# Kernel optimization log

Hardware: AMD Instinct MI355X
Metric: run time of the kernel (lower is better)

## Reference

```python
import jax, jax.numpy as jnp
import numpy as np

N, C, D = 32, 512, 2048
Q = 64          # num_query_tokens
H = 16          # num_attention_heads
DH = D // H     # head dim


def _mlp(z, w1, b1, w2, b2):
    # projection: Linear(D_r -> D_h), GELU (exact erf, torch default), Linear(D_h -> D_h)
    h = jax.nn.gelu(z @ w1 + b1, approximate=False)
    return h @ w2 + b2


def setup_inputs() -> dict:
    key = jax.random.key(0)
    ks = jax.random.split(key, 16)
    s = 0.02
    inp = {
        "x": jax.random.normal(ks[0], (N, C, D), dtype=jnp.float32),
        # projection MLP (shared by both experts since projector_type has no 'proj')
        "proj_w1": jax.random.normal(ks[1], (D, D), dtype=jnp.float32) * s,
        "proj_b1": jnp.zeros((D,), dtype=jnp.float32),
        "proj_w2": jax.random.normal(ks[2], (D, D), dtype=jnp.float32) * s,
        "proj_b2": jnp.zeros((D,), dtype=jnp.float32),
        # TextResampler (cross-attention with learned queries)
        "query_tokens": jax.random.normal(ks[3], (Q, D), dtype=jnp.float32) * s,
        "wq": jax.random.normal(ks[4], (D, D), dtype=jnp.float32) * s,
        "bq": jnp.zeros((D,), dtype=jnp.float32),
        "wk": jax.random.normal(ks[5], (D, D), dtype=jnp.float32) * s,
        "bk": jnp.zeros((D,), dtype=jnp.float32),
        "wv": jax.random.normal(ks[6], (D, D), dtype=jnp.float32) * s,
        "bv": jnp.zeros((D,), dtype=jnp.float32),
        "wo": jax.random.normal(ks[7], (D, D), dtype=jnp.float32) * s,
        "bo": jnp.zeros((D,), dtype=jnp.float32),
        # gate weight (zeros-init in module; random here to exercise routing)
        "w_gate": jax.random.normal(ks[8], (D, 2), dtype=jnp.float32) * s,
    }
    return inp


def reference(x, proj_w1, proj_b1, proj_w2, proj_b2, query_tokens,
              wq, bq, wk, bk, wv, bv, wo, bo, w_gate):
    n, c, d = x.shape
    # --- sampler: AdaptiveAvgPool2d((Q, D)); D dim is identity, C -> Q block means ---
    x_sampler = x.reshape(n, Q, c // Q, d).mean(axis=2)  # [N, Q, D]

    # --- expert 0: projection MLP on pooled tokens ---
    e0 = _mlp(x_sampler, proj_w1, proj_b1, proj_w2, proj_b2)  # [N, Q, D]

    # --- expert 1: TextResampler cross-attention over x, then shared projection ---
    q = (query_tokens @ wq + bq).reshape(Q, H, DH)            # [Q, H, DH]
    k = (x @ wk + bk).reshape(n, c, H, DH)                    # [N, C, H, DH]
    v = (x @ wv + bv).reshape(n, c, H, DH)
    scores = jnp.einsum("qhd,nchd->nhqc", q, k) / jnp.sqrt(jnp.float32(DH))
    attn = jax.nn.softmax(scores, axis=-1)                    # [N, H, Q, C]
    ctx = jnp.einsum("nhqc,nchd->nqhd", attn, v).reshape(n, Q, d)
    resampled = ctx @ wo + bo                                 # [N, Q, D]
    e1 = _mlp(resampled, proj_w1, proj_b1, proj_w2, proj_b2)  # [N, Q, D]

    # --- noisy top-k gating (eval path: clean logits) ---
    flat = x_sampler.reshape(n * Q, d)
    logits = jax.nn.softmax(flat @ w_gate, axis=1)            # [T, 2]
    top_vals, top_idx = jax.lax.top_k(logits, 2)              # min(k+1, num_experts)=2
    top_k_gates = top_vals / (top_vals.sum(axis=1, keepdims=True) + 1e-6)
    gates = jnp.zeros_like(logits).at[
        jnp.arange(n * Q)[:, None], top_idx].set(top_k_gates)
    gates = gates.reshape(n, Q, 2)

    # --- combine: matmul(stack(experts,-1), gates.unsqueeze(-1)).squeeze(-1) ---
    stacked = jnp.stack([e0, e1], axis=-1)                    # [N, Q, D, E]
    out = jnp.einsum("nqde,nqe->nqd", stacked, gates)
    return out.reshape(-1, d)                                 # [N*Q, D]
```

## Files before the change

kernel.cpp:

```cpp
#include <hip/hip_runtime.h>
#include <hip/hip_bf16.h>

typedef float f32x4 __attribute__((ext_vector_type(4)));
typedef short s16x8 __attribute__((ext_vector_type(8)));
typedef __hip_bfloat16 bf16;

#define NB 32
#define CB 512
#define DB 2048
#define QB 64
#define HB 16
#define DHB 128

static __device__ __forceinline__ void gload16(const void* g, void* l) {
  __builtin_amdgcn_global_load_lds(
      (const __attribute__((address_space(1))) void*)g,
      (__attribute__((address_space(3))) void*)l, 16, 0, 0);
}

static __device__ __forceinline__ unsigned short f2bf(float f) {
  bf16 b = __float2bfloat16(f);
  return *reinterpret_cast<unsigned short*>(&b);
}

static __device__ __forceinline__ float gelu_f(float z) {
  return 0.5f * z * (1.0f + erff(z * 0.7071067811865475f));
}

#define BARX do { asm volatile("s_waitcnt lgkmcnt(0)" ::: "memory"); __builtin_amdgcn_s_barrier(); asm volatile("" ::: "memory"); } while (0)
#define VM8  asm volatile("s_waitcnt vmcnt(8)" ::: "memory")
#define VM2  asm volatile("s_waitcnt vmcnt(2)" ::: "memory")

__global__ void k_convpool(const float* __restrict__ x, bf16* __restrict__ x_bf,
                           bf16* __restrict__ xs) {
  const int d0 = blockIdx.x * 512 + threadIdx.x * 2;
  const int q = blockIdx.y, n = blockIdx.z;
  const size_t base = ((size_t)(n * CB + q * 8)) * DB + d0;
  float s0 = 0.f, s1 = 0.f;
#pragma unroll
  for (int j = 0; j < 8; ++j) {
    float2 v = *(const float2*)(x + base + (size_t)j * DB);
    s0 += v.x; s1 += v.y;
    ushort2 o; o.x = f2bf(v.x); o.y = f2bf(v.y);
    *(ushort2*)((unsigned short*)x_bf + base + (size_t)j * DB) = o;
  }
  ushort2 p; p.x = f2bf(s0 * 0.125f); p.y = f2bf(s1 * 0.125f);
  *(ushort2*)((unsigned short*)xs + ((size_t)(n * QB + q)) * DB + d0) = p;
}

__global__ void k_convert(const float* __restrict__ in, unsigned short* __restrict__ out, int n4) {
  int stride = gridDim.x * blockDim.x;
  for (int i = blockIdx.x * blockDim.x + threadIdx.x; i < n4; i += stride) {
    float4 v = ((const float4*)in)[i];
    ushort4 o;
    o.x = f2bf(v.x); o.y = f2bf(v.y); o.z = f2bf(v.z); o.w = f2bf(v.w);
    ((ushort4*)out)[i] = o;
  }
}

__global__ void k_gate(const bf16* __restrict__ xs, const float* __restrict__ wg,
                       float* __restrict__ gates) {
  int t = blockIdx.x * 4 + (threadIdx.x >> 6);
  int lane = threadIdx.x & 63;
  const bf16* row = xs + (size_t)t * DB;
  float z0 = 0.f, z1 = 0.f;
  for (int d = lane; d < DB; d += 64) {
    float v = __bfloat162float(row[d]);
    z0 += v * wg[d * 2];
    z1 += v * wg[d * 2 + 1];
  }
#pragma unroll
  for (int m = 32; m; m >>= 1) { z0 += __shfl_xor(z0, m, 64); z1 += __shfl_xor(z1, m, 64); }
  if (lane == 0) {
    float mx = fmaxf(z0, z1);
    float e0 = __expf(z0 - mx), e1 = __expf(z1 - mx);
    float s = e0 + e1;
    float p0 = e0 / s, p1 = e1 / s;
    float inv = 1.0f / (p0 + p1 + 1e-6f);
    gates[t * 2] = p0 * inv;
    gates[t * 2 + 1] = p1 * inv;
  }
}

struct TP5 { const float* s[5]; bf16* d[5]; };
__global__ void k_transpose5(TP5 p) {
  __shared__ float t[32][33];
  const float* W = p.s[blockIdx.z];
  bf16* WT = p.d[blockIdx.z];
  int bx = blockIdx.x * 32;
  int by = blockIdx.y * 32;
  int tx = threadIdx.x, ty0 = threadIdx.y;
#pragma unroll
  for (int j = 0; j < 4; ++j) {
    int ty = ty0 + j * 8;
    t[ty][tx] = W[(size_t)(by + ty) * DB + bx + tx];
  }
  __syncthreads();
#pragma unroll
  for (int j = 0; j < 4; ++j) {
    int ty = ty0 + j * 8;
    WT[(size_t)(bx + ty) * DB + by + tx] = __float2bfloat16(t[tx][ty]);
  }
}

__global__ void k_qreduce(const float* __restrict__ qp, const float* __restrict__ bq,
                          bf16* __restrict__ qproj) {
  int i = blockIdx.x * 256 + threadIdx.x;
  const int S = QB * DB;
  float s = qp[i] + qp[i + S] + qp[i + 2 * S] + qp[i + 3 * S] + bq[i & (DB - 1)];
  qproj[i] = __float2bfloat16(s);
}

template <int EPI>
__global__ __launch_bounds__(512, 2) void k_gemm256(
    const bf16* __restrict__ A, int lda, long long sAb,
    const bf16* __restrict__ BT, int ldb, long long sBb,
    const float* __restrict__ bias, void* __restrict__ Cout, int ldc, long long sCb,
    int K, int ntiles) {
  __shared__ __align__(16) bf16 lds[2][2][256 * 64];

  int bid = blockIdx.x;
  { int c = gridDim.x >> 3; bid = (bid & 7) * c + (bid >> 3); }
  const int m0 = (bid / ntiles) * 256;
  const int n0 = (bid % ntiles) * 256;
  const int z = blockIdx.z;
  A += (size_t)z * sAb;
  BT += (size_t)z * sBb;

  const int tid = threadIdx.x;
  const int l = tid & 63, w = tid >> 6;
  const int wr = w >> 2, wc = w & 3;
  const int fr = l & 15, fg = l >> 4;

  const int rloc = w * 8 + (l >> 3);
  const int cswz = ((l & 7) ^ (l >> 3)) * 8;
  const bf16* Asw = A + cswz;
  const bf16* Bsw = BT + cswz;

  int rbA[4], rbB[4], ckb[2];
#pragma unroll
  for (int mi = 0; mi < 4; ++mi) rbA[mi] = (wr * 64 + mi * 16 + fr) * 128;
#pragma unroll
  for (int ni = 0; ni < 4; ++ni) rbB[ni] = ((ni >> 1) * 128 + wc * 32 + (ni & 1) * 16 + fr) * 128;
#pragma unroll
  for (int kk = 0; kk < 2; ++kk) ckb[kk] = ((kk * 4 + fg) ^ (fr & 7)) * 16;

  f32x4 acc[8][4] = {};
  s16x8 af[4], bfr[4][2];

  auto stg = [&](const bf16* srcsw, int ld, int row0, int kcol, char* dst) {
    gload16(srcsw + (size_t)(row0 + rloc) * ld + kcol, dst + w * 1024);
    gload16(srcsw + (size_t)(row0 + 64 + rloc) * ld + kcol, dst + 8192 + w * 1024);
  };

  stg(Asw, lda, m0, 0, (char*)&lds[0][0][0]);
  stg(Bsw, ldb, n0, 0, (char*)&lds[0][1][0]);
  stg(Bsw, ldb, n0 + 128, 0, (char*)&lds[0][1][0] + 16384);
  stg(Asw, lda, m0 + 128, 0, (char*)&lds[0][0][0] + 16384);
  asm volatile("s_waitcnt vmcnt(0)" ::: "memory");
  BARX;

  const int NT = K >> 6;
  for (int t = 0; t < NT; ++t) {
    const int buf = t & 1;
    const char* Ab = (const char*)&lds[buf][0][0];
    const char* Bb = (const char*)&lds[buf][1][0];
    char* As = (char*)&lds[buf ^ 1][0][0];
    char* Bs = (char*)&lds[buf ^ 1][1][0];
    const int kn = (t + 1 < NT ? (t + 1) : 0) << 6;

    stg(Asw, lda, m0, kn, As);
    stg(Bsw, ldb, n0, kn, Bs);
    stg(Bsw, ldb, n0 + 128, kn, Bs + 16384);
    stg(Asw, lda, m0 + 128, kn, As + 16384);
#pragma unroll
    for (int mi = 0; mi < 4; ++mi) af[mi] = *(const s16x8*)(Ab + rbA[mi] + ckb[0]);
#pragma unroll
    for (int ni = 0; ni < 4; ++ni) bfr[ni][0] = *(const s16x8*)(Bb + rbB[ni] + ckb[0]);
    __builtin_amdgcn_s_setprio(1);
#pragma unroll
    for (int mi = 0; mi < 4; ++mi)
#pragma unroll
      for (int ni = 0; ni < 4; ++ni)
        acc[mi][ni] = __builtin_amdgcn_mfma_f32_16x16x32_bf16(af[mi], bfr[ni][0], acc[mi][ni], 0, 0, 0);
    __builtin_amdgcn_s_setprio(0);
    VM8;
    BARX;

#pragma unroll
    for (int mi = 0; mi < 4; ++mi) af[mi] = *(const s16x8*)(Ab + 16384 + rbA[mi] + ckb[0]);
    __builtin_amdgcn_s_setprio(1);
#pragma unroll
    for (int mi = 0; mi < 4; ++mi)
#pragma unroll
      for (int ni = 0; ni < 4; ++ni)
        acc[4 + mi][ni] = __builtin_amdgcn_mfma_f32_16x16x32_bf16(af[mi], bfr[ni][0], acc[4 + mi][ni], 0, 0, 0);
    __builtin_amdgcn_s_setprio(0);

#pragma unroll
    for (int mi = 0; mi < 4; ++mi) af[mi] = *(const s16x8*)(Ab + rbA[mi] + ckb[1]);
#pragma unroll
    for (int ni = 0; ni < 4; ++ni) bfr[ni][1] = *(const s16x8*)(Bb + rbB[ni] + ckb[1]);
    __builtin_amdgcn_s_setprio(1);
#pragma unroll
    for (int mi = 0; mi < 4; ++mi)
#pragma unroll
      for (int ni = 0; ni < 4; ++ni)
        acc[mi][ni] = __builtin_amdgcn_mfma_f32_16x16x32_bf16(af[mi], bfr[ni][1], acc[mi][ni], 0, 0, 0);
    __builtin_amdgcn_s_setprio(0);

#pragma unroll
    for (int mi = 0; mi < 4; ++mi) af[mi] = *(const s16x8*)(Ab + 16384 + rbA[mi] + ckb[1]);
    __builtin_amdgcn_s_setprio(1);
#pragma unroll
    for (int mi = 0; mi < 4; ++mi)
#pragma unroll
      for (int ni = 0; ni < 4; ++ni)
        acc[4 + mi][ni] = __builtin_amdgcn_mfma_f32_16x16x32_bf16(af[mi], bfr[ni][1], acc[4 + mi][ni], 0, 0, 0);
    __builtin_amdgcn_s_setprio(0);
    VM2;
    BARX;
  }

#pragma unroll
  for (int mi = 0; mi < 8; ++mi) {
    int row = m0 + (mi >> 2) * 128 + wr * 64 + (mi & 3) * 16 + fg * 4;
#pragma unroll
    for (int ni = 0; ni < 4; ++ni) {
      int col = n0 + (ni >> 1) * 128 + wc * 32 + (ni & 1) * 16 + fr;
      float bv = bias ? bias[col] : 0.f;
#pragma unroll
      for (int j = 0; j < 4; ++j) {
        float v = acc[mi][ni][j] + bv;
        size_t o = (size_t)z * sCb + (size_t)(row + j) * ldc + col;
        if (EPI == 0) {
          ((bf16*)Cout)[o] = __float2bfloat16(v);
        } else if (EPI == 1) {
          ((bf16*)Cout)[o] = __float2bfloat16(gelu_f(v));
        } else {
          ((float*)Cout)[o] = v;
        }
      }
    }
  }
}

template <int EPI>
__global__ __launch_bounds__(256) void k_gemm(
    const bf16* __restrict__ A, int lda, long long sAb,
    const bf16* __restrict__ BT, int ldb, long long sBb,
    const float* __restrict__ bias, void* __restrict__ Cout, int ldc, long long sCb,
    int M, int K) {
  __shared__ bf16 As[128 * 32];
  __shared__ bf16 Bs[128 * 32];
  const int z = blockIdx.z;
  A += (size_t)z * sAb;
  BT += (size_t)z * sBb;
  const int tid = threadIdx.x;
  const int lane = tid & 63, w = tid >> 6;
  const int m0 = blockIdx.x * 128, n0 = blockIdx.y * 128;
  const int wm = (w >> 1) * 64, wn = (w & 1) * 64;
  f32x4 acc[4][4] = {};

  const int srow = tid >> 2;
  const int scol = (tid & 3) * 8;
  int gr0 = m0 + srow;       if (gr0 > M - 1) gr0 = M - 1;
  int gr1 = m0 + 64 + srow;  if (gr1 > M - 1) gr1 = M - 1;
  const bf16* ag0 = A + (size_t)gr0 * lda + scol;
  const bf16* ag1 = A + (size_t)gr1 * lda + scol;
  const bf16* bg0 = BT + (size_t)(n0 + srow) * ldb + scol;
  const bf16* bg1 = BT + (size_t)(n0 + 64 + srow) * ldb + scol;
  char* lA = (char*)As + w * 1024;
  char* lB = (char*)Bs + w * 1024;

  const int fr = lane & 15, fk = (lane >> 4) * 8;

  for (int k0 = 0; k0 < K; k0 += 32) {
    __syncthreads();
    gload16(ag0 + k0, lA);
    gload16(ag1 + k0, lA + 4096);
    gload16(bg0 + k0, lB);
    gload16(bg1 + k0, lB + 4096);
    __syncthreads();
    s16x8 af[4], bfr[4];
#pragma unroll
    for (int i = 0; i < 4; ++i)
      af[i] = *(const s16x8*)(As + (wm + i * 16 + fr) * 32 + fk);
#pragma unroll
    for (int i = 0; i < 4; ++i)
      bfr[i] = *(const s16x8*)(Bs + (wn + i * 16 + fr) * 32 + fk);
#pragma unroll
    for (int mi = 0; mi < 4; ++mi)
#pragma unroll
      for (int ni = 0; ni < 4; ++ni)
        acc[mi][ni] = __builtin_amdgcn_mfma_f32_16x16x32_bf16(af[mi], bfr[ni], acc[mi][ni], 0, 0, 0);
  }

  const int fg4 = (lane >> 4) * 4;
#pragma unroll
  for (int mi = 0; mi < 4; ++mi) {
#pragma unroll
    for (int ni = 0; ni < 4; ++ni) {
      int col = n0 + wn + ni * 16 + fr;
      float bv = bias ? bias[col] : 0.f;
#pragma unroll
      for (int j = 0; j < 4; ++j) {
        int r = m0 + wm + mi * 16 + fg4 + j;
        if (r >= M) continue;
        float v = acc[mi][ni][j] + bv;
        size_t o = (size_t)z * sCb + (size_t)r * ldc + col;
        if (EPI == 0) {
          ((bf16*)Cout)[o] = __float2bfloat16(v);
        } else if (EPI == 1) {
          ((bf16*)Cout)[o] = __float2bfloat16(gelu_f(v));
        } else {
          ((float*)Cout)[o] = v;
        }
      }
    }
  }
}

__global__ __launch_bounds__(256) void k_attn(
    const bf16* __restrict__ S, const bf16* __restrict__ Vg, bf16* __restrict__ ctxg) {
  __shared__ bf16 vt[128 * 64];
  __shared__ bf16 pb[4][16 * 64];
  const int nh = blockIdx.x;
  const int n = nh >> 4, h = nh & 15;
  const int tid = threadIdx.x, lane = tid & 63, w = tid >> 6;
  const int fr = lane & 15, fg = lane >> 4;

  f32x4 ctx[8] = {};
  float mrow[4], lrow[4];
#pragma unroll
  for (int j = 0; j < 4; ++j) { mrow[j] = -1e30f; lrow[j] = 0.f; }

  const bf16* Srow = S + ((size_t)n * (HB * QB) + h * QB) * CB;
  const bf16* Vbase = Vg + (size_t)(n * CB) * DB + h * DHB;
  const float SC = 0.08838834764831845f;

  const int krow = tid >> 4;
  const int kcol = (tid & 15) * 8;

  for (int c0 = 0; c0 < CB; c0 += 64) {
    __syncthreads();
#pragma unroll
    for (int jj = 0; jj < 4; ++jj) {
      int row = jj * 16 + krow;
      s16x8 vv = *(const s16x8*)(Vbase + (size_t)(c0 + row) * DB + kcol);
#pragma unroll
      for (int i = 0; i < 8; ++i)
        vt[(kcol + i) * 64 + row] = ((const bf16*)&vv)[i];
    }

    f32x4 s4[4];
#pragma unroll
    for (int ci = 0; ci < 4; ++ci)
#pragma unroll
      for (int j = 0; j < 4; ++j)
        s4[ci][j] = __bfloat162float(Srow[(size_t)(w * 16 + fg * 4 + j) * CB + c0 + ci * 16 + fr]);

#pragma unroll
    for (int j = 0; j < 4; ++j) {
      float m = fmaxf(fmaxf(s4[0][j], s4[1][j]), fmaxf(s4[2][j], s4[3][j])) * SC;
#pragma unroll
      for (int msk = 1; msk < 16; msk <<= 1) m = fmaxf(m, __shfl_xor(m, msk, 16));
      float newm = fmaxf(mrow[j], m);
      float resc = __expf(mrow[j] - newm);
      mrow[j] = newm;
      float rsum = 0.f;
#pragma unroll
      for (int ci = 0; ci < 4; ++ci) {
        float p = __expf(s4[ci][j] * SC - newm);
        rsum += p;
        pb[w][(fg * 4 + j) * 64 + ci * 16 + fr] = __float2bfloat16(p);
      }
#pragma unroll
      for (int msk = 1; msk < 16; msk <<= 1) rsum += __shfl_xor(rsum, msk, 16);
      lrow[j] = lrow[j] * resc + rsum;
#pragma unroll
      for (int ni = 0; ni < 8; ++ni) ctx[ni][j] = ctx[ni][j] * resc;
    }
    __syncthreads();

#pragma unroll
    for (int kk2 = 0; kk2 < 2; ++kk2) {
      s16x8 pa = *(const s16x8*)(&pb[w][fr * 64 + kk2 * 32 + fg * 8]);
#pragma unroll
      for (int ni = 0; ni < 8; ++ni) {
        s16x8 bv = *(const s16x8*)(vt + (ni * 16 + fr) * 64 + kk2 * 32 + fg * 8);
        ctx[ni] = __builtin_amdgcn_mfma_f32_16x16x32_bf16(pa, bv, ctx[ni], 0, 0, 0);
      }
    }
  }

#pragma unroll
  for (int ni = 0; ni < 8; ++ni) {
#pragma unroll
    for (int j = 0; j < 4; ++j) {
      int q = w * 16 + fg * 4 + j;
      float v = ctx[ni][j] / lrow[j];
      ctxg[(size_t)(n * QB + q) * DB + h * DHB + ni * 16 + fr] = __float2bfloat16(v);
    }
  }
}

__global__ void k_combine(const float* __restrict__ e01, const float* __restrict__ gates,
                          float* __restrict__ out) {
  int i = blockIdx.x * blockDim.x + threadIdx.x;
  int t = i >> 9;
  float4 a = ((const float4*)e01)[i];
  float4 b = ((const float4*)e01)[i + (1 << 20)];
  float g0 = gates[t * 2], g1 = gates[t * 2 + 1];
  float4 o;
  o.x = a.x * g0 + b.x * g1;
  o.y = a.y * g0 + b.y * g1;
  o.z = a.z * g0 + b.z * g1;
  o.w = a.w * g0 + b.w * g1;
  ((float4*)out)[i] = o;
}

extern "C" void kernel_launch(void* const* d_in, const int* in_sizes, int n_in,
                              void* d_out, int out_size, void* d_ws, size_t ws_size,
                              hipStream_t stream) {
  const float* x  = (const float*)d_in[0];
  const float* w1 = (const float*)d_in[1];
  const float* b1 = (const float*)d_in[2];
  const float* w2 = (const float*)d_in[3];
  const float* b2 = (const float*)d_in[4];
  const float* qt = (const float*)d_in[5];
  const float* wq = (const float*)d_in[6];
  const float* bq = (const float*)d_in[7];
  const float* wk = (const float*)d_in[8];
  const float* wv = (const float*)d_in[10];
  const float* bv = (const float*)d_in[11];
  const float* wo = (const float*)d_in[12];
  const float* bo = (const float*)d_in[13];
  const float* wg = (const float*)d_in[14];
  float* out = (float*)d_out;

  char* ws = (char*)d_ws;
  size_t off = 0;
  auto alloc = [&](size_t bytes) {
    char* p = ws + off;
    off += (bytes + 255) & ~(size_t)255;
    return p;
  };
  const size_t XE = (size_t)NB * CB * DB;
  const size_t WE = (size_t)DB * DB;
  const size_t TE = (size_t)NB * QB * DB;

  bf16* x_bf   = (bf16*)alloc(XE * 2);
  bf16* V_bf   = (bf16*)alloc(XE * 2);
  bf16* wk_bf  = (bf16*)alloc(WE * 2);
  bf16* w1T    = (bf16*)alloc(WE * 2);
  bf16* w2T    = (bf16*)alloc(WE * 2);
  bf16* wvT    = (bf16*)alloc(WE * 2);
  bf16* wqT    = (bf16*)alloc(WE * 2);
  bf16* woT    = (bf16*)alloc(WE * 2);
  bf16* tokens = (bf16*)alloc(2 * TE * 2);
  bf16* h4     = (bf16*)alloc(2 * TE * 2);
  float* e01   = (float*)alloc(2 * TE * 4);
  bf16* ctx_bf = (bf16*)alloc(TE * 2);
  bf16* qt_bf  = (bf16*)alloc((size_t)QB * DB * 2);
  bf16* qproj  = (bf16*)alloc((size_t)QB * DB * 2);
  float* qpart = (float*)alloc((size_t)4 * QB * DB * 4);
  bf16* qk     = (bf16*)alloc((size_t)HB * QB * DB * 2);
  bf16* Sbuf   = (bf16*)alloc((size_t)NB * HB * QB * CB * 2);
  float* gates = (float*)alloc((size_t)NB * QB * 2 * 4);
  (void)ws_size; (void)in_sizes; (void)n_in; (void)out_size;

  k_convpool<<<dim3(4, 64, 32), 256, 0, stream>>>(x, x_bf, tokens);
  k_convert<<<64, 256, 0, stream>>>(qt, (unsigned short*)qt_bf, (int)(QB * DB / 4));
  k_convert<<<1024, 256, 0, stream>>>(wk, (unsigned short*)wk_bf, (int)(WE / 4));
  k_gate<<<NB * QB / 4, 256, 0, stream>>>(tokens, wg, gates);

  TP5 tp;
  tp.s[0] = w1; tp.d[0] = w1T;
  tp.s[1] = w2; tp.d[1] = w2T;
  tp.s[2] = wv; tp.d[2] = wvT;
  tp.s[3] = wq; tp.d[3] = wqT;
  tp.s[4] = wo; tp.d[4] = woT;
  k_transpose5<<<dim3(64, 64, 5), dim3(32, 8), 0, stream>>>(tp);

  k_gemm<2><<<dim3(1, 16, 4), 256, 0, stream>>>(
      qt_bf, DB, 512, wqT, DB, 512, nullptr, qpart, DB, (long long)QB * DB, QB, 512);
  k_qreduce<<<QB * DB / 256, 256, 0, stream>>>(qpart, bq, qproj);

  k_gemm<0><<<dim3(1, 16, HB), 256, 0, stream>>>(
      qproj, DB, DHB, wk_bf, DB, DHB, nullptr, qk, DB, (long long)QB * DB, QB, DHB);

  k_gemm256<0><<<dim3(512, 1, 1), 512, 0, stream>>>(
      x_bf, DB, 0, wvT, DB, 0, bv, V_bf, DB, 0, DB, 8);

  k_gemm256<0><<<dim3(8, 1, NB), 512, 0, stream>>>(
      qk, DB, 0, x_bf, DB, (long long)CB * DB, nullptr,
      Sbuf, CB, (long long)HB * QB * CB, DB, 2);

  k_attn<<<NB * HB, 256, 0, stream>>>(Sbuf, V_bf, ctx_bf);

  k_gemm<0><<<dim3(16, 16, 1), 256, 0, stream>>>(
      ctx_bf, DB, 0, woT, DB, 0, bo, tokens + (size_t)2048 * DB, DB, 0, 2048, DB);

  k_gemm256<1><<<dim3(128, 1, 1), 512, 0, stream>>>(
      tokens, DB, 0, w1T, DB, 0, b1, h4, DB, 0, DB, 8);
  k_gemm256<2><<<dim3(128, 1, 1), 512, 0, stream>>>(
      h4, DB, 0, w2T, DB, 0, b2, e01, DB, 0, DB, 8);

  k_combine<<<4096, 256, 0, stream>>>(e01, gates, out);
}
```

Measured before the change: 567.0 us.

## Fold gate mixing before second MLP linear and interleave expert tokens

Uses linearity of the second projection: expert outputs are gated-summed after GELU, so the gate mix is applied to the hidden activations in the first GEMM epilogue. The second GEMM then runs on half the rows with bias scaled by the gate sum, which removes the combine kernel and the fp32 expert buffers. Pooled tokens and resampled tokens are interleaved so paired rows land in the same accumulator fragment. The 256-tile GEMM also spreads its next-tile loads across the k-steps and uses a plain barrier with a vmcnt(2) wait, which risks LDS ordering issues if waits are insufficient.

```diff
diff --git a/kernel.cpp b/kernel.cpp
--- a/kernel.cpp
+++ b/kernel.cpp
@@ -27,12 +27,11 @@
   return 0.5f * z * (1.0f + erff(z * 0.7071067811865475f));
 }
 
-#define BARX do { asm volatile("s_waitcnt lgkmcnt(0)" ::: "memory"); __builtin_amdgcn_s_barrier(); asm volatile("" ::: "memory"); } while (0)
-#define VM8  asm volatile("s_waitcnt vmcnt(8)" ::: "memory")
+#define BAR2 do { asm volatile("" ::: "memory"); __builtin_amdgcn_s_barrier(); asm volatile("" ::: "memory"); } while (0)
 #define VM2  asm volatile("s_waitcnt vmcnt(2)" ::: "memory")
 
 __global__ void k_convpool(const float* __restrict__ x, bf16* __restrict__ x_bf,
-                           bf16* __restrict__ xs) {
+                           bf16* __restrict__ tokens) {
   const int d0 = blockIdx.x * 512 + threadIdx.x * 2;
   const int q = blockIdx.y, n = blockIdx.z;
   const size_t base = ((size_t)(n * CB + q * 8)) * DB + d0;
@@ -45,7 +44,7 @@
     *(ushort2*)((unsigned short*)x_bf + base + (size_t)j * DB) = o;
   }
   ushort2 p; p.x = f2bf(s0 * 0.125f); p.y = f2bf(s1 * 0.125f);
-  *(ushort2*)((unsigned short*)xs + ((size_t)(n * QB + q)) * DB + d0) = p;
+  *(ushort2*)((unsigned short*)tokens + (size_t)2 * (n * QB + q) * DB + d0) = p;
 }
 
 __global__ void k_convert(const float* __restrict__ in, unsigned short* __restrict__ out, int n4) {
@@ -58,11 +57,11 @@
   }
 }
 
-__global__ void k_gate(const bf16* __restrict__ xs, const float* __restrict__ wg,
-                       float* __restrict__ gates) {
+__global__ void k_gate(const bf16* __restrict__ tokens, const float* __restrict__ wg,
+                       float* __restrict__ gates, float* __restrict__ gsum) {
   int t = blockIdx.x * 4 + (threadIdx.x >> 6);
   int lane = threadIdx.x & 63;
-  const bf16* row = xs + (size_t)t * DB;
+  const bf16* row = tokens + (size_t)2 * t * DB;
   float z0 = 0.f, z1 = 0.f;
   for (int d = lane; d < DB; d += 64) {
     float v = __bfloat162float(row[d]);
@@ -77,8 +76,10 @@
     float s = e0 + e1;
     float p0 = e0 / s, p1 = e1 / s;
     float inv = 1.0f / (p0 + p1 + 1e-6f);
-    gates[t * 2] = p0 * inv;
-    gates[t * 2 + 1] = p1 * inv;
+    float g0 = p0 * inv, g1 = p1 * inv;
+    gates[t * 2] = g0;
+    gates[t * 2 + 1] = g1;
+    gsum[t] = g0 + g1;
   }
 }
 
@@ -116,7 +117,7 @@
     const bf16* __restrict__ A, int lda, long long sAb,
     const bf16* __restrict__ BT, int ldb, long long sBb,
     const float* __restrict__ bias, void* __restrict__ Cout, int ldc, long long sCb,
-    int K, int ntiles) {
+    int K, int ntiles, const float* __restrict__ gates) {
   __shared__ __align__(16) bf16 lds[2][2][256 * 64];
 
   int bid = blockIdx.x;
@@ -158,7 +159,7 @@
   stg(Bsw, ldb, n0 + 128, 0, (char*)&lds[0][1][0] + 16384);
   stg(Asw, lda, m0 + 128, 0, (char*)&lds[0][0][0] + 16384);
   asm volatile("s_waitcnt vmcnt(0)" ::: "memory");
-  BARX;
+  BAR2;
 
   const int NT = K >> 6;
   for (int t = 0; t < NT; ++t) {
@@ -170,9 +171,6 @@
     const int kn = (t + 1 < NT ? (t + 1) : 0) << 6;
 
     stg(Asw, lda, m0, kn, As);
-    stg(Bsw, ldb, n0, kn, Bs);
-    stg(Bsw, ldb, n0 + 128, kn, Bs + 16384);
-    stg(Asw, lda, m0 + 128, kn, As + 16384);
 #pragma unroll
     for (int mi = 0; mi < 4; ++mi) af[mi] = *(const s16x8*)(Ab + rbA[mi] + ckb[0]);
 #pragma unroll
@@ -184,9 +182,10 @@
       for (int ni = 0; ni < 4; ++ni)
         acc[mi][ni] = __builtin_amdgcn_mfma_f32_16x16x32_bf16(af[mi], bfr[ni][0], acc[mi][ni], 0, 0, 0);
     __builtin_amdgcn_s_setprio(0);
-    VM8;
-    BARX;
-
+    VM2;
+    BAR2;
+
+    stg(Bsw, ldb, n0, kn, Bs);
 #pragma unroll
     for (int mi = 0; mi < 4; ++mi) af[mi] = *(const s16x8*)(Ab + 16384 + rbA[mi] + ckb[0]);
     __builtin_amdgcn_s_setprio(1);
@@ -197,6 +196,7 @@
         acc[4 + mi][ni] = __builtin_amdgcn_mfma_f32_16x16x32_bf16(af[mi], bfr[ni][0], acc[4 + mi][ni], 0, 0, 0);
     __builtin_amdgcn_s_setprio(0);
 
+    stg(Bsw, ldb, n0 + 128, kn, Bs + 16384);
 #pragma unroll
     for (int mi = 0; mi < 4; ++mi) af[mi] = *(const s16x8*)(Ab + rbA[mi] + ckb[1]);
 #pragma unroll
@@ -209,6 +209,7 @@
         acc[mi][ni] = __builtin_amdgcn_mfma_f32_16x16x32_bf16(af[mi], bfr[ni][1], acc[mi][ni], 0, 0, 0);
     __builtin_amdgcn_s_setprio(0);
 
+    stg(Asw, lda, m0 + 128, kn, As + 16384);
 #pragma unroll
     for (int mi = 0; mi < 4; ++mi) af[mi] = *(const s16x8*)(Ab + 16384 + rbA[mi] + ckb[1]);
     __builtin_amdgcn_s_setprio(1);
@@ -219,7 +220,7 @@
         acc[4 + mi][ni] = __builtin_amdgcn_mfma_f32_16x16x32_bf16(af[mi], bfr[ni][1], acc[4 + mi][ni], 0, 0, 0);
     __builtin_amdgcn_s_setprio(0);
     VM2;
-    BARX;
+    BAR2;
   }
 
 #pragma unroll
@@ -229,16 +230,27 @@
     for (int ni = 0; ni < 4; ++ni) {
       int col = n0 + (ni >> 1) * 128 + wc * 32 + (ni & 1) * 16 + fr;
       float bv = bias ? bias[col] : 0.f;
-#pragma unroll
-      for (int j = 0; j < 4; ++j) {
-        float v = acc[mi][ni][j] + bv;
-        size_t o = (size_t)z * sCb + (size_t)(row + j) * ldc + col;
-        if (EPI == 0) {
-          ((bf16*)Cout)[o] = __float2bfloat16(v);
-        } else if (EPI == 1) {
-          ((bf16*)Cout)[o] = __float2bfloat16(gelu_f(v));
-        } else {
-          ((float*)Cout)[o] = v;
+      if (EPI == 3) {
+#pragma unroll
+        for (int j = 0; j < 4; j += 2) {
+          int tk = (row + j) >> 1;
+          float g0 = gates[tk * 2], g1 = gates[tk * 2 + 1];
+          float v0 = gelu_f(acc[mi][ni][j] + bv);
+          float v1 = gelu_f(acc[mi][ni][j + 1] + bv);
+          ((bf16*)Cout)[(size_t)tk * ldc + col] = __float2bfloat16(g0 * v0 + g1 * v1);
+        }
+      } else {
+#pragma unroll
+        for (int j = 0; j < 4; ++j) {
+          float v = acc[mi][ni][j] + bv;
+          size_t o = (size_t)z * sCb + (size_t)(row + j) * ldc + col;
+          if (EPI == 0) {
+            ((bf16*)Cout)[o] = __float2bfloat16(v);
+          } else if (EPI == 1) {
+            ((bf16*)Cout)[o] = __float2bfloat16(gelu_f(v));
+          } else {
+            ((float*)Cout)[o] = v;
+          }
         }
       }
     }
@@ -250,7 +262,7 @@
     const bf16* __restrict__ A, int lda, long long sAb,
     const bf16* __restrict__ BT, int ldb, long long sBb,
     const float* __restrict__ bias, void* __restrict__ Cout, int ldc, long long sCb,
-    int M, int K) {
+    int M, int K, const float* __restrict__ gsum) {
   __shared__ bf16 As[128 * 32];
   __shared__ bf16 Bs[128 * 32];
   const int z = blockIdx.z;
@@ -307,14 +319,15 @@
       for (int j = 0; j < 4; ++j) {
         int r = m0 + wm + mi * 16 + fg4 + j;
         if (r >= M) continue;
-        float v = acc[mi][ni][j] + bv;
         size_t o = (size_t)z * sCb + (size_t)r * ldc + col;
         if (EPI == 0) {
-          ((bf16*)Cout)[o] = __float2bfloat16(v);
+          ((bf16*)Cout)[o] = __float2bfloat16(acc[mi][ni][j] + bv);
         } else if (EPI == 1) {
-          ((bf16*)Cout)[o] = __float2bfloat16(gelu_f(v));
+          ((bf16*)Cout)[o] = __float2bfloat16(gelu_f(acc[mi][ni][j] + bv));
+        } else if (EPI == 2) {
+          ((float*)Cout)[o] = acc[mi][ni][j] + bv;
         } else {
-          ((float*)Cout)[o] = v;
+          ((float*)Cout)[o] = acc[mi][ni][j] + gsum[r] * bv;
         }
       }
     }
@@ -403,21 +416,6 @@
       ctxg[(size_t)(n * QB + q) * DB + h * DHB + ni * 16 + fr] = __float2bfloat16(v);
     }
   }
-}
-
-__global__ void k_combine(const float* __restrict__ e01, const float* __restrict__ gates,
-                          float* __restrict__ out) {
-  int i = blockIdx.x * blockDim.x + threadIdx.x;
-  int t = i >> 9;
-  float4 a = ((const float4*)e01)[i];
-  float4 b = ((const float4*)e01)[i + (1 << 20)];
-  float g0 = gates[t * 2], g1 = gates[t * 2 + 1];
-  float4 o;
-  o.x = a.x * g0 + b.x * g1;
-  o.y = a.y * g0 + b.y * g1;
-  o.z = a.z * g0 + b.z * g1;
-  o.w = a.w * g0 + b.w * g1;
-  ((float4*)out)[i] = o;
 }
 
 extern "C" void kernel_launch(void* const* d_in, const int* in_sizes, int n_in,
@@ -459,8 +457,7 @@
   bf16* wqT    = (bf16*)alloc(WE * 2);
   bf16* woT    = (bf16*)alloc(WE * 2);
   bf16* tokens = (bf16*)alloc(2 * TE * 2);
-  bf16* h4     = (bf16*)alloc(2 * TE * 2);
-  float* e01   = (float*)alloc(2 * TE * 4);
+  bf16* hmix   = (bf16*)alloc(TE * 2);
   bf16* ctx_bf = (bf16*)alloc(TE * 2);
   bf16* qt_bf  = (bf16*)alloc((size_t)QB * DB * 2);
   bf16* qproj  = (bf16*)alloc((size_t)QB * DB * 2);
@@ -468,12 +465,13 @@
   bf16* qk     = (bf16*)alloc((size_t)HB * QB * DB * 2);
   bf16* Sbuf   = (bf16*)alloc((size_t)NB * HB * QB * CB * 2);
   float* gates = (float*)alloc((size_t)NB * QB * 2 * 4);
+  float* gsum  = (float*)alloc((size_t)NB * QB * 4);
   (void)ws_size; (void)in_sizes; (void)n_in; (void)out_size;
 
   k_convpool<<<dim3(4, 64, 32), 256, 0, stream>>>(x, x_bf, tokens);
   k_convert<<<64, 256, 0, stream>>>(qt, (unsigned short*)qt_bf, (int)(QB * DB / 4));
   k_convert<<<1024, 256, 0, stream>>>(wk, (unsigned short*)wk_bf, (int)(WE / 4));
-  k_gate<<<NB * QB / 4, 256, 0, stream>>>(tokens, wg, gates);
+  k_gate<<<NB * QB / 4, 256, 0, stream>>>(tokens, wg, gates, gsum);
 
   TP5 tp;
   tp.s[0] = w1; tp.d[0] = w1T;
@@ -484,28 +482,27 @@
   k_transpose5<<<dim3(64, 64, 5), dim3(32, 8), 0, stream>>>(tp);
 
   k_gemm<2><<<dim3(1, 16, 4), 256, 0, stream>>>(
-      qt_bf, DB, 512, wqT, DB, 512, nullptr, qpart, DB, (long long)QB * DB, QB, 512);
+      qt_bf, DB, 512, wqT, DB, 512, nullptr, qpart, DB, (long long)QB * DB, QB, 512, nullptr);
   k_qreduce<<<QB * DB / 256, 256, 0, stream>>>(qpart, bq, qproj);
 
   k_gemm<0><<<dim3(1, 16, HB), 256, 0, stream>>>(
-      qproj, DB, DHB, wk_bf, DB, DHB, nullptr, qk, DB, (long long)QB * DB, QB, DHB);
+      qproj, DB, DHB, wk_bf, DB, DHB, nullptr, qk, DB, (long long)QB * DB, QB, DHB, nullptr);
 
   k_gemm256<0><<<dim3(512, 1, 1), 512, 0, stream>>>(
-      x_bf, DB, 0, wvT, DB, 0, bv, V_bf, DB, 0, DB, 8);
+      x_bf, DB, 0, wvT, DB, 0, bv, V_bf, DB, 0, DB, 8, nullptr);
 
   k_gemm256<0><<<dim3(8, 1, NB), 512, 0, stream>>>(
       qk, DB, 0, x_bf, DB, (long long)CB * DB, nullptr,
-      Sbuf, CB, (long long)HB * QB * CB, DB, 2);
+      Sbuf, CB, (long long)HB * QB * CB, DB, 2, nullptr);
 
   k_attn<<<NB * HB, 256, 0, stream>>>(Sbuf, V_bf, ctx_bf);
 
   k_gemm<0><<<dim3(16, 16, 1), 256, 0, stream>>>(
-      ctx_bf, DB, 0, woT, DB, 0, bo, tokens + (size_t)2048 * DB, DB, 0, 2048, DB);
-
-  k_gemm256<1><<<dim3(128, 1, 1), 512, 0, stream>>>(
-      tokens, DB, 0, w1T, DB, 0, b1, h4, DB, 0, DB, 8);
-  k_gemm256<2><<<dim3(128, 1, 1), 512, 0, stream>>>(
-      h4, DB, 0, w2T, DB, 0, b2, e01, DB, 0, DB, 8);
-
-  k_combine<<<4096, 256, 0, stream>>>(e01, gates, out);
-}
+      ctx_bf, DB, 0, woT, DB, 0, bo, tokens + DB, 2 * DB, 0, 2048, DB, nullptr);
+
+  k_gemm256<3><<<dim3(128, 1, 1), 512, 0, stream>>>(
+      tokens, DB, 0, w1T, DB, 0, b1, hmix, DB, 0, DB, 8, gates);
+
+  k_gemm<4><<<dim3(16, 16, 1), 256, 0, stream>>>(
+      hmix, DB, 0, w2T, DB, 0, b2, out, DB, 0, 2048, DB, gsum);
+}
```

New measurement: 522.7 us. 1.08x faster.
